# Kernel tuning notes

Measured on AMD Instinct MI355X. Metric: run time of the kernel, lower is better.

Reference implementation:

```python
import math
import jax, jax.numpy as jnp
import numpy as np

B, S, D, H, FF = 2, 2048, 1024, 16, 4096
HD = D // H  # head dim = 64
EPS = 1e-12


def setup_inputs() -> dict:
    key = jax.random.key(0)
    ks = jax.random.split(key, 16)
    w = lambda k, shape: (jax.random.normal(k, shape, jnp.float32) * 0.02)
    return {
        "hidden_states": jax.random.normal(ks[0], (B, S, D), jnp.float32),
        "attention_mask": jnp.zeros((B, 1, 1, S), jnp.float32),
        "wq": w(ks[1], (D, D)), "bq": jnp.zeros((D,), jnp.float32),
        "wk": w(ks[2], (D, D)), "bk": jnp.zeros((D,), jnp.float32),
        "wv": w(ks[3], (D, D)), "bv": jnp.zeros((D,), jnp.float32),
        "wo": w(ks[4], (D, D)), "bo": jnp.zeros((D,), jnp.float32),
        "w1": w(ks[5], (D, FF)), "b1": jnp.zeros((FF,), jnp.float32),
        "w2": w(ks[6], (FF, D)), "b2": jnp.zeros((D,), jnp.float32),
        "g1": jnp.ones((D,), jnp.float32), "be1": jnp.zeros((D,), jnp.float32),
        "g2": jnp.ones((D,), jnp.float32), "be2": jnp.zeros((D,), jnp.float32),
    }


def _layernorm(x, g, b):
    mu = jnp.mean(x, axis=-1, keepdims=True)
    var = jnp.mean(jnp.square(x - mu), axis=-1, keepdims=True)
    return (x - mu) * jax.lax.rsqrt(var + EPS) * g + b


def _gelu_erf(x):
    # x * 0.5 * (1 + erf(x / sqrt(2)))  -- exact erf gelu as in source
    return x * 0.5 * (1.0 + jax.lax.erf(x / math.sqrt(2.0)))


def _attention(x, mask, wq, bq, wk, bk, wv, bv, wo, bo):
    b, s, d = x.shape
    split = lambda t: t.reshape(b, s, H, HD).transpose(0, 2, 1, 3)  # [b,h,s,hd]
    q = split(x @ wq + bq)
    k = split(x @ wk + bk)
    v = split(x @ wv + bv)
    scores = jnp.einsum("bhqd,bhkd->bhqk", q, k) / math.sqrt(HD)
    scores = scores + mask  # broadcast [b,1,1,s]
    probs = jax.nn.softmax(scores, axis=-1)
    ctx = jnp.einsum("bhqk,bhkd->bhqd", probs, v)
    ctx = ctx.transpose(0, 2, 1, 3).reshape(b, s, d)
    return ctx @ wo + bo


def reference(hidden_states, attention_mask, wq, bq, wk, bk, wv, bv, wo, bo,
              w1, b1, w2, b2, g1, be1, g2, be2):
    # prenorm transformer layer (dropout = identity in eval)
    residual = hidden_states
    h = _layernorm(hidden_states, g1, be1)
    attn = _attention(h, attention_mask, wq, bq, wk, bk, wv, bv, wo, bo)
    h = residual + attn
    residual = h
    h2 = _layernorm(h, g2, be2)
    ff = _gelu_erf(h2 @ w1 + b1) @ w2 + b2
    return residual + ff
```

## Files before the change

kernel.cpp:

```cpp
#include <hip/hip_runtime.h>
#include <hip/hip_bf16.h>
#include <math.h>


#define BB 2
#define SS 2048
#define DD 1024
#define HH 16
#define HDIM 64
#define FFD 4096
#define NTOK (BB*SS)
#define LOG2E 1.4426950408889634f

typedef __attribute__((ext_vector_type(8))) short bf16x8;
typedef __attribute__((ext_vector_type(4))) float f32x4;
typedef __attribute__((ext_vector_type(16))) float f32x16;
typedef __attribute__((ext_vector_type(4))) unsigned int u32x4;

#if __has_builtin(__builtin_amdgcn_exp2f)
#define EXP2(x) __builtin_amdgcn_exp2f(x)
#else
#define EXP2(x) exp2f(x)
#endif

__device__ __forceinline__ void gl_lds16(const void* g, void* l) {
  __builtin_amdgcn_global_load_lds(
      (const __attribute__((address_space(1))) unsigned int*)g,
      (__attribute__((address_space(3))) unsigned int*)l, 16, 0, 0);
}

__device__ __forceinline__ short f2bf(float f) {
  unsigned int u = __builtin_bit_cast(unsigned int, f);
  unsigned int r = (u + 0x7fffu + ((u >> 16) & 1u)) >> 16;
  return (short)r;
}
__device__ __forceinline__ float bf2f(short s) {
  return __builtin_bit_cast(float, ((unsigned)(unsigned short)s) << 16);
}
__device__ __forceinline__ unsigned pk2(float lo, float hi) {
  unsigned r;
  asm("v_cvt_pk_bf16_f32 %0, %1, %2" : "=v"(r) : "v"(lo), "v"(hi));
  return r;
}

__global__ __launch_bounds__(256) void convT(const float* __restrict__ w,
                                             __hip_bfloat16* __restrict__ wt,
                                             int K, int N) {
  __shared__ float tile[32][33];
  int k0 = blockIdx.y * 32, n0 = blockIdx.x * 32;
  int tx = threadIdx.x & 31, ty = threadIdx.x >> 5;
#pragma unroll
  for (int i = 0; i < 4; ++i) {
    int r = ty + i * 8;
    tile[r][tx] = w[(size_t)(k0 + r) * N + n0 + tx];
  }
  __syncthreads();
#pragma unroll
  for (int i = 0; i < 4; ++i) {
    int r = ty + i * 8;
    wt[(size_t)(n0 + r) * K + k0 + tx] = __float2bfloat16(tile[tx][r]);
  }
}

__global__ __launch_bounds__(256) void ln_bf16(const float* __restrict__ x,
                                               const float* __restrict__ g,
                                               const float* __restrict__ be,
                                               __hip_bfloat16* __restrict__ out) {
  int w = threadIdx.x >> 6, lane = threadIdx.x & 63;
  int row = blockIdx.x * 4 + w;
  const float* xr = x + (size_t)row * DD;
  float4 v[4];
  float sum = 0.f, sq = 0.f;
#pragma unroll
  for (int i = 0; i < 4; ++i) {
    v[i] = *(const float4*)(xr + lane * 4 + i * 256);
    sum += v[i].x + v[i].y + v[i].z + v[i].w;
    sq += v[i].x * v[i].x + v[i].y * v[i].y + v[i].z * v[i].z + v[i].w * v[i].w;
  }
#pragma unroll
  for (int off = 1; off < 64; off <<= 1) {
    sum += __shfl_xor(sum, off);
    sq += __shfl_xor(sq, off);
  }
  float mu = sum * (1.f / 1024.f);
  float var = sq * (1.f / 1024.f) - mu * mu;
  float rs = rsqrtf(var + 1e-12f);
  __hip_bfloat16* orow = out + (size_t)row * DD;
#pragma unroll
  for (int i = 0; i < 4; ++i) {
    int c = lane * 4 + i * 256;
    float4 gg = *(const float4*)(g + c);
    float4 bb = *(const float4*)(be + c);
    short4 o;
    o.x = f2bf((v[i].x - mu) * rs * gg.x + bb.x);
    o.y = f2bf((v[i].y - mu) * rs * gg.y + bb.y);
    o.z = f2bf((v[i].z - mu) * rs * gg.z + bb.z);
    o.w = f2bf((v[i].w - mu) * rs * gg.w + bb.w);
    *(short4*)((short*)orow + c) = o;
  }
}

template <int EPI>
__global__ __launch_bounds__(256, 4) void gemm_bt(
    const __hip_bfloat16* __restrict__ A, const __hip_bfloat16* __restrict__ BT,
    const float* __restrict__ bA, const float* __restrict__ bB,
    const float* __restrict__ bC,
    void* __restrict__ C0, void* __restrict__ C1, void* __restrict__ C2,
    int M, int N, int K, int kSplit) {
  __shared__ __align__(16) char smem[34816];
  short* As = (short*)smem;
  short* Bs = (short*)(smem + 8192);
  const int t = threadIdx.x, lane = t & 63, w = t >> 6;
  const int m0 = blockIdx.y * 128, n0 = blockIdx.x * 128;
  const int wm = (w >> 1) * 64, wn = (w & 1) * 64;
  const int row16 = lane & 15, grp = lane >> 4;
  const int arow = t >> 2, achunk = t & 3;
  f32x4 acc[4][4] = {};

  const int steps = K >> 5;
  const int z = blockIdx.z;
  const int sBeg = (z * steps) / kSplit, sEnd = ((z + 1) * steps) / kSplit;

  for (int s = sBeg; s < sEnd; ++s) {
    const int kt = s << 5;
    __syncthreads();
#pragma unroll
    for (int j = 0; j < 2; ++j) {
      int r = arow + j * 64;
      gl_lds16(A + (size_t)(m0 + r) * K + kt + achunk * 8,
               (char*)As + r * 64 + achunk * 16);
      gl_lds16(BT + (size_t)(n0 + r) * K + kt + achunk * 8,
               (char*)Bs + r * 64 + achunk * 16);
    }
    __syncthreads();
    bf16x8 af[4], bfr[4];
#pragma unroll
    for (int f = 0; f < 4; ++f) {
      af[f] = *(const bf16x8*)((const char*)As + (wm + f * 16 + row16) * 64 + grp * 16);
      bfr[f] = *(const bf16x8*)((const char*)Bs + (wn + f * 16 + row16) * 64 + grp * 16);
    }
#pragma unroll
    for (int mf = 0; mf < 4; ++mf)
#pragma unroll
      for (int nf = 0; nf < 4; ++nf)
        acc[mf][nf] =
            __builtin_amdgcn_mfma_f32_16x16x32_bf16(af[mf], bfr[nf], acc[mf][nf], 0, 0, 0);
  }

  __syncthreads();

  if constexpr (EPI == 5) {
    if (n0 >= 2048) {
#pragma unroll
      for (int nf = 0; nf < 4; ++nf) {
        int vloc = wn + nf * 16 + row16;
        float bv = bC[n0 - 2048 + vloc];
#pragma unroll
        for (int mf = 0; mf < 4; ++mf) {
          int tloc = wm + mf * 16 + grp * 4;
          f32x4 a = acc[mf][nf];
          *(uint2*)(smem + vloc * 272 + tloc * 2) =
              make_uint2(pk2(a[0] + bv, a[1] + bv), pk2(a[2] + bv, a[3] + bv));
        }
      }
      __syncthreads();
      int vrBase = ((m0 >> 11) << 10) + (n0 - 2048);
      int mcol = m0 & 2047;
#pragma unroll
      for (int i = 0; i < 8; ++i) {
        int c = t + i * 256;
        int vr = c >> 4, tc = c & 15;
        u32x4 vv = *(const u32x4*)(smem + vr * 272 + tc * 16);
        *(u32x4*)((__hip_bfloat16*)C2 + (size_t)(vrBase + vr) * 2048 + mcol + tc * 8) = vv;
      }
      return;
    }
  }

  __hip_bfloat16* outP = nullptr;
  int ldO = N, colB = n0;
  const float* bp = nullptr;
  if constexpr (EPI == 1) { outP = (__hip_bfloat16*)C0; bp = bA; }
  if constexpr (EPI == 5) {
    const bool isK = n0 >= 1024;
    outP = (__hip_bfloat16*)(isK ? C1 : C0);
    bp = isK ? bB : bA;
    ldO = 1024; colB = n0 & 1023;
  }
  if constexpr (EPI == 7) outP = (__hip_bfloat16*)C0 + (size_t)z * 4194304ull;
  if constexpr (EPI == 8)
    outP = (__hip_bfloat16*)C0 + ((z == 0) ? 0ull : ((z == 1) ? 4194304ull : 12582912ull));

#pragma unroll
  for (int nf = 0; nf < 4; ++nf) {
    int nn = wn + nf * 16 + row16;
    float bv = bp ? bp[colB + nn] : 0.f;
#pragma unroll
    for (int mf = 0; mf < 4; ++mf) {
      int mloc = wm + mf * 16 + grp * 4;
      f32x4 a = acc[mf][nf];
#pragma unroll
      for (int r = 0; r < 4; ++r) {
        float v = a[r] + bv;
        if constexpr (EPI == 1)
          v = 0.5f * v * (1.0f + erff(v * 0.70710678118654752f));
        *(short*)(smem + (mloc + r) * 272 + nn * 2) = f2bf(v);
      }
    }
  }
  __syncthreads();
#pragma unroll
  for (int i = 0; i < 8; ++i) {
    int c = t + i * 256;
    int mmr = c >> 4, nc = c & 15;
    u32x4 vv = *(const u32x4*)(smem + mmr * 272 + nc * 16);
    *(u32x4*)(outP + (size_t)(m0 + mmr) * ldO + colB + nc * 8) = vv;
  }
}

__global__ __launch_bounds__(256) void reduce3(const __hip_bfloat16* __restrict__ p0,
                                               const __hip_bfloat16* __restrict__ p1,
                                               const __hip_bfloat16* __restrict__ p2,
                                               const float* __restrict__ h1,
                                               const float* __restrict__ b2,
                                               float* __restrict__ out) {
  int idx = (blockIdx.x * 256 + threadIdx.x) * 8;
  int n = idx & 1023;
  bf16x8 a = *(const bf16x8*)(p0 + idx);
  bf16x8 b = *(const bf16x8*)(p1 + idx);
  bf16x8 c = *(const bf16x8*)(p2 + idx);
  float4 hA = *(const float4*)(h1 + idx), hB = *(const float4*)(h1 + idx + 4);
  float4 bA = *(const float4*)(b2 + n), bB = *(const float4*)(b2 + n + 4);
  float o[8];
#pragma unroll
  for (int j = 0; j < 8; ++j) o[j] = bf2f(a[j]) + bf2f(b[j]) + bf2f(c[j]);
  float4 r0 = make_float4(o[0] + hA.x + bA.x, o[1] + hA.y + bA.y,
                          o[2] + hA.z + bA.z, o[3] + hA.w + bA.w);
  float4 r1 = make_float4(o[4] + hB.x + bB.x, o[5] + hB.y + bB.y,
                          o[6] + hB.z + bB.z, o[7] + hB.w + bB.w);
  *(float4*)(out + idx) = r0;
  *(float4*)(out + idx + 4) = r1;
}

__global__ __launch_bounds__(256) void reduce4(const __hip_bfloat16* __restrict__ p0,
                                               const __hip_bfloat16* __restrict__ p1,
                                               const __hip_bfloat16* __restrict__ p2,
                                               const __hip_bfloat16* __restrict__ p3,
                                               const float* __restrict__ x,
                                               const float* __restrict__ bo,
                                               float* __restrict__ out) {
  int idx = (blockIdx.x * 256 + threadIdx.x) * 8;
  int n = idx & 1023;
  bf16x8 a = *(const bf16x8*)(p0 + idx);
  bf16x8 b = *(const bf16x8*)(p1 + idx);
  bf16x8 c = *(const bf16x8*)(p2 + idx);
  bf16x8 d = *(const bf16x8*)(p3 + idx);
  float4 hA = *(const float4*)(x + idx), hB = *(const float4*)(x + idx + 4);
  float4 bA = *(const float4*)(bo + n), bB = *(const float4*)(bo + n + 4);
  float o[8];
#pragma unroll
  for (int j = 0; j < 8; ++j)
    o[j] = (bf2f(a[j]) + bf2f(b[j])) + (bf2f(c[j]) + bf2f(d[j]));
  float4 r0 = make_float4(o[0] + hA.x + bA.x, o[1] + hA.y + bA.y,
                          o[2] + hA.z + bA.z, o[3] + hA.w + bA.w);
  float4 r1 = make_float4(o[4] + hB.x + bB.x, o[5] + hB.y + bB.y,
                          o[6] + hB.z + bB.z, o[7] + hB.w + bB.w);
  *(float4*)(out + idx) = r0;
  *(float4*)(out + idx + 4) = r1;
}

__global__ __launch_bounds__(512) void flash_attn2(
    const __hip_bfloat16* __restrict__ Q,
    const __hip_bfloat16* __restrict__ Kg,
    const __hip_bfloat16* __restrict__ VTg,
    const float* __restrict__ mask,
    __hip_bfloat16* __restrict__ pctx0,
    __hip_bfloat16* __restrict__ pctx1,
    float2* __restrict__ ml) {
  __shared__ __align__(16) char lds[33280];
  const int t = threadIdx.x, lane = t & 63, w = t >> 6;
  const int l31 = lane & 31, hi = lane >> 5;
  const int q0 = blockIdx.x * 256;
  const int bh = blockIdx.y, b = bh >> 4, h = bh & 15;
  const int z = blockIdx.z;
  const int kvBase = z * (SS / 2);
  __hip_bfloat16* pctx = z ? pctx1 : pctx0;
  const int qrow = q0 + w * 32 + l31;

  bf16x8 qf[4];
  {
    const __hip_bfloat16* qp = Q + ((size_t)(b * SS + qrow)) * DD + h * HDIM + hi * 8;
    qf[0] = *(const bf16x8*)(qp);
    qf[1] = *(const bf16x8*)(qp + 16);
    qf[2] = *(const bf16x8*)(qp + 32);
    qf[3] = *(const bf16x8*)(qp + 48);
  }
  f32x16 ctx0 = {}, ctx1 = {};
  float m = -1e30f, l = 0.f, mC = -1.44e30f;

  auto stage = [&](int buf, int kv0) {
    int r = t >> 3, c = t & 7;
    gl_lds16(Kg + ((size_t)(b * SS + kv0 + r)) * DD + h * HDIM + ((c ^ (r & 7)) * 8),
             lds + buf * 8192 + t * 16);
    gl_lds16(VTg + ((size_t)(bh * 64 + r)) * 2048 + kv0 + ((c ^ (r & 7)) * 8),
             lds + 16384 + buf * 8192 + t * 16);
    if (t < 64) *(float*)(lds + 32768 + buf * 256 + t * 4) = mask[b * SS + kv0 + t];
  };

  stage(0, kvBase);
  const int NIT = SS / 128;
  for (int it = 0; it < NIT; ++it) {
    __syncthreads();
    if (it + 1 < NIT) stage((it + 1) & 1, kvBase + (it + 1) * 64);
    const char* Kb = lds + (it & 1) * 8192;
    const char* Vb = lds + 16384 + (it & 1) * 8192;
    const float* mk = (const float*)(lds + 32768 + (it & 1) * 256);

    f32x16 s0 = {}, s1 = {};
#pragma unroll
    for (int kc = 0; kc < 4; ++kc) {
      int c = kc * 2 + hi;
      int r0 = l31, r1 = 32 + l31;
      bf16x8 ka0 = *(const bf16x8*)(Kb + r0 * 128 + ((c ^ (r0 & 7)) << 4));
      bf16x8 ka1 = *(const bf16x8*)(Kb + r1 * 128 + ((c ^ (r1 & 7)) << 4));
      s0 = __builtin_amdgcn_mfma_f32_32x32x16_bf16(ka0, qf[kc], s0, 0, 0, 0);
      s1 = __builtin_amdgcn_mfma_f32_32x32x16_bf16(ka1, qf[kc], s1, 0, 0, 0);
    }
#pragma unroll
    for (int g = 0; g < 4; ++g) {
      float4 mg0 = *(const float4*)(mk + g * 8 + hi * 4);
      float4 mg1 = *(const float4*)(mk + 32 + g * 8 + hi * 4);
      const float* m0p = (const float*)&mg0;
      const float* m1p = (const float*)&mg1;
#pragma unroll
      for (int i = 0; i < 4; ++i) {
        s0[g * 4 + i] = fmaf(s0[g * 4 + i], 0.125f, m0p[i]);
        s1[g * 4 + i] = fmaf(s1[g * 4 + i], 0.125f, m1p[i]);
      }
    }
    float pmax;
    {
      f32x16 q8;
#pragma unroll
      for (int r = 0; r < 16; ++r) q8[r] = fmaxf(s0[r], s1[r]);
#pragma unroll
      for (int r = 0; r < 8; ++r) q8[r] = fmaxf(q8[r], q8[r + 8]);
#pragma unroll
      for (int r = 0; r < 4; ++r) q8[r] = fmaxf(q8[r], q8[r + 4]);
      pmax = fmaxf(fmaxf(q8[0], q8[1]), fmaxf(q8[2], q8[3]));
      pmax = fmaxf(pmax, __shfl_xor(pmax, 32));
    }
    if (__any(pmax > m + 8.0f)) {
      float mnew = fmaxf(m, pmax);
      float fac = EXP2((m - mnew) * LOG2E);
      l *= fac;
#pragma unroll
      for (int r = 0; r < 16; ++r) { ctx0[r] *= fac; ctx1[r] *= fac; }
      m = mnew;
      mC = m * LOG2E;
    }
    float rsA = 0.f, rsB = 0.f;
#pragma unroll
    for (int r = 0; r < 16; ++r) {
      s0[r] = EXP2(fmaf(s0[r], LOG2E, -mC));
      s1[r] = EXP2(fmaf(s1[r], LOG2E, -mC));
      rsA += s0[r];
      rsB += s1[r];
    }
    rsA += rsB;
    rsA += __shfl_xor(rsA, 32);
    l += rsA;

    unsigned W0[8], W1[8];
#pragma unroll
    for (int g = 0; g < 4; ++g) {
      W0[g * 2] = pk2(s0[g * 4 + 0], s0[g * 4 + 1]);
      W0[g * 2 + 1] = pk2(s0[g * 4 + 2], s0[g * 4 + 3]);
      W1[g * 2] = pk2(s1[g * 4 + 0], s1[g * 4 + 1]);
      W1[g * 2 + 1] = pk2(s1[g * 4 + 2], s1[g * 4 + 3]);
    }
    unsigned swA0 = __shfl_xor(hi ? W0[0] : W0[2], 32);
    unsigned swA1 = __shfl_xor(hi ? W0[1] : W0[3], 32);
    unsigned swB0 = __shfl_xor(hi ? W0[4] : W0[6], 32);
    unsigned swB1 = __shfl_xor(hi ? W0[5] : W0[7], 32);
    unsigned swC0 = __shfl_xor(hi ? W1[0] : W1[2], 32);
    unsigned swC1 = __shfl_xor(hi ? W1[1] : W1[3], 32);
    unsigned swD0 = __shfl_xor(hi ? W1[4] : W1[6], 32);
    unsigned swD1 = __shfl_xor(hi ? W1[5] : W1[7], 32);
    u32x4 pb[4];
    pb[0] = hi ? (u32x4){swA0, swA1, W0[2], W0[3]} : (u32x4){W0[0], W0[1], swA0, swA1};
    pb[1] = hi ? (u32x4){swB0, swB1, W0[6], W0[7]} : (u32x4){W0[4], W0[5], swB0, swB1};
    pb[2] = hi ? (u32x4){swC0, swC1, W1[2], W1[3]} : (u32x4){W1[0], W1[1], swC0, swC1};
    pb[3] = hi ? (u32x4){swD0, swD1, W1[6], W1[7]} : (u32x4){W1[4], W1[5], swD0, swD1};

#pragma unroll
    for (int kc = 0; kc < 4; ++kc) {
      bf16x8 pbf = __builtin_bit_cast(bf16x8, pb[kc]);
      int c = kc * 2 + hi;
      int r0 = l31, r1 = 32 + l31;
      bf16x8 va0 = *(const bf16x8*)(Vb + r0 * 128 + ((c ^ (r0 & 7)) << 4));
      bf16x8 va1 = *(const bf16x8*)(Vb + r1 * 128 + ((c ^ (r1 & 7)) << 4));
      ctx0 = __builtin_amdgcn_mfma_f32_32x32x16_bf16(va0, pbf, ctx0, 0, 0, 0);
      ctx1 = __builtin_amdgcn_mfma_f32_32x32x16_bf16(va1, pbf, ctx1, 0, 0, 0);
    }
  }

  if (hi == 0) ml[((size_t)z * NTOK + b * SS + qrow) * HH + h] = make_float2(m, l);

  __syncthreads();
  {
    int row = w * 32 + l31;
#pragma unroll
    for (int dt = 0; dt < 2; ++dt) {
#pragma unroll
      for (int g = 0; g < 4; ++g) {
        unsigned lo2 = dt ? pk2(ctx1[g * 4 + 0], ctx1[g * 4 + 1]) : pk2(ctx0[g * 4 + 0], ctx0[g * 4 + 1]);
        unsigned hi2 = dt ? pk2(ctx1[g * 4 + 2], ctx1[g * 4 + 3]) : pk2(ctx0[g * 4 + 2], ctx0[g * 4 + 3]);
        int c = dt * 4 + g;
        *(uint2*)(lds + row * 128 + ((c ^ (row & 7)) << 4) + hi * 8) = make_uint2(lo2, hi2);
      }
    }
  }
  __syncthreads();
  {
    int r = t >> 1;
    size_t tok = (size_t)(b * SS + q0 + r);
#pragma unroll
    for (int i = 0; i < 4; ++i) {
      int c = (t & 1) * 4 + i;
      u32x4 vv = *(const u32x4*)(lds + r * 128 + ((c ^ (r & 7)) << 4));
      *(u32x4*)((short*)pctx + tok * DD + h * HDIM + c * 8) = vv;
    }
  }
}

__global__ __launch_bounds__(256) void mergeAttn(
    const __hip_bfloat16* __restrict__ p0, const __hip_bfloat16* __restrict__ p1,
    const float2* __restrict__ ml, __hip_bfloat16* __restrict__ out) {
  int tok = blockIdx.x, tid = threadIdx.x;
  int h = tid >> 4;
  float2 a = ml[(size_t)tok * HH + h];
  float2 b = ml[(size_t)(NTOK + tok) * HH + h];
  float M = fmaxf(a.x, b.x);
  float w0 = EXP2((a.x - M) * LOG2E), w1 = EXP2((b.x - M) * LOG2E);
  float inv = 1.0f / (w0 * a.y + w1 * b.y);
  w0 *= inv; w1 *= inv;
  size_t idx = (size_t)tok * DD + tid * 4;
  short4 c0 = *(const short4*)((const short*)p0 + idx);
  short4 c1 = *(const short4*)((const short*)p1 + idx);
  unsigned lo = pk2(w0 * bf2f(c0.x) + w1 * bf2f(c1.x),
                    w0 * bf2f(c0.y) + w1 * bf2f(c1.y));
  unsigned hi2 = pk2(w0 * bf2f(c0.z) + w1 * bf2f(c1.z),
                     w0 * bf2f(c0.w) + w1 * bf2f(c1.w));
  *(uint2*)((short*)out + idx) = make_uint2(lo, hi2);
}

extern "C" void kernel_launch(void* const* d_in, const int* in_sizes, int n_in,
                              void* d_out, int out_size, void* d_ws, size_t ws_size,
                              hipStream_t stream) {
  const float* x = (const float*)d_in[0];
  const float* mask = (const float*)d_in[1];
  const float* wq = (const float*)d_in[2];
  const float* bq = (const float*)d_in[3];
  const float* wk = (const float*)d_in[4];
  const float* bk = (const float*)d_in[5];
  const float* wv = (const float*)d_in[6];
  const float* bv = (const float*)d_in[7];
  const float* wo = (const float*)d_in[8];
  const float* bo = (const float*)d_in[9];
  const float* w1 = (const float*)d_in[10];
  const float* b1 = (const float*)d_in[11];
  const float* w2 = (const float*)d_in[12];
  const float* b2 = (const float*)d_in[13];
  const float* g1 = (const float*)d_in[14];
  const float* be1 = (const float*)d_in[15];
  const float* g2 = (const float*)d_in[16];
  const float* be2 = (const float*)d_in[17];

  char* ws = (char*)d_ws;
  const size_t MB = 1024ull * 1024ull;
  __hip_bfloat16* wqkvT = (__hip_bfloat16*)(ws + 0 * MB);
  __hip_bfloat16* woT = (__hip_bfloat16*)(ws + 6 * MB);
  __hip_bfloat16* w1T = (__hip_bfloat16*)(ws + 8 * MB);
  __hip_bfloat16* w2T = (__hip_bfloat16*)(ws + 16 * MB);
  __hip_bfloat16* xn = (__hip_bfloat16*)(ws + 24 * MB);
  __hip_bfloat16* qb = (__hip_bfloat16*)(ws + 32 * MB);
  __hip_bfloat16* kb = (__hip_bfloat16*)(ws + 40 * MB);
  __hip_bfloat16* vtb = (__hip_bfloat16*)(ws + 48 * MB);
  __hip_bfloat16* ctxb = (__hip_bfloat16*)(ws + 56 * MB);
  float* h1 = (float*)(ws + 64 * MB);
  __hip_bfloat16* h2 = xn;
  __hip_bfloat16* a1 = qb;
  __hip_bfloat16* pctx0 = (__hip_bfloat16*)(ws + 24 * MB);
  __hip_bfloat16* pctx1 = (__hip_bfloat16*)(ws + 64 * MB);
  float2* mlbuf = (float2*)(ws + 72 * MB);

  convT<<<dim3(32, 32), 256, 0, stream>>>(wq, wqkvT, 1024, 1024);
  convT<<<dim3(32, 32), 256, 0, stream>>>(wk, wqkvT + 1024 * 1024, 1024, 1024);
  convT<<<dim3(32, 32), 256, 0, stream>>>(wv, wqkvT + 2 * 1024 * 1024, 1024, 1024);
  convT<<<dim3(32, 32), 256, 0, stream>>>(wo, woT, 1024, 1024);
  convT<<<dim3(128, 32), 256, 0, stream>>>(w1, w1T, 1024, 4096);
  convT<<<dim3(32, 128), 256, 0, stream>>>(w2, w2T, 4096, 1024);

  ln_bf16<<<1024, 256, 0, stream>>>(x, g1, be1, xn);

  gemm_bt<5><<<dim3(24, 32), 256, 0, stream>>>(
      xn, wqkvT, bq, bk, bv, qb, kb, vtb, NTOK, 3072, 1024, 1);

  flash_attn2<<<dim3(8, 32, 2), 512, 0, stream>>>(qb, kb, vtb, mask,
                                                  pctx0, pctx1, mlbuf);
  mergeAttn<<<4096, 256, 0, stream>>>(pctx0, pctx1, mlbuf, ctxb);

  gemm_bt<7><<<dim3(8, 32, 4), 256, 0, stream>>>(
      ctxb, woT, nullptr, nullptr, nullptr, ws + 24 * MB, nullptr, nullptr,
      NTOK, 1024, 1024, 4);

  reduce4<<<2048, 256, 0, stream>>>((__hip_bfloat16*)(ws + 24 * MB),
                                    (__hip_bfloat16*)(ws + 32 * MB),
                                    (__hip_bfloat16*)(ws + 40 * MB),
                                    (__hip_bfloat16*)(ws + 48 * MB),
                                    x, bo, h1);

  ln_bf16<<<1024, 256, 0, stream>>>(h1, g2, be2, h2);

  gemm_bt<1><<<dim3(32, 32), 256, 0, stream>>>(
      h2, w1T, b1, nullptr, nullptr, a1, nullptr, nullptr, NTOK, FFD, 1024, 1);

  gemm_bt<8><<<dim3(8, 32, 3), 256, 0, stream>>>(
      a1, w2T, nullptr, nullptr, nullptr, ws, nullptr, nullptr,
      NTOK, 1024, FFD, 3);

  reduce3<<<2048, 256, 0, stream>>>((__hip_bfloat16*)(ws + 0 * MB),
                                    (__hip_bfloat16*)(ws + 8 * MB),
                                    (__hip_bfloat16*)(ws + 24 * MB),
                                    h1, b2, (float*)d_out);
}
```

Baseline: 287.9 us.

## Triple-buffer GEMM LDS tiles with async global-to-LDS prefetch two stages ahead

Replaces the single-buffered GEMM main loop (sync, load, sync, compute) with a three-stage LDS ring buffer. Global-to-LDS loads for tile t+2 are issued before the MFMAs of tile t, with explicit vmcnt waits and a single barrier per iteration. The aim is to hide global memory latency behind the matrix math and halve the barriers. In exchange LDS per block grows to 48KB and launch bounds drop to 3 blocks per CU, which lowers occupancy.

```diff
diff --git a/kernel.cpp b/kernel.cpp
--- a/kernel.cpp
+++ b/kernel.cpp
@@ -22,6 +22,12 @@
 #else
 #define EXP2(x) exp2f(x)
 #endif
+
+#define BAR __builtin_amdgcn_s_barrier
+#define SCB __builtin_amdgcn_sched_barrier
+#define VM4 asm volatile("s_waitcnt vmcnt(4)" ::: "memory")
+#define VM0 asm volatile("s_waitcnt vmcnt(0)" ::: "memory")
+#define LGK0 asm volatile("s_waitcnt lgkmcnt(0)" ::: "memory")
 
 __device__ __forceinline__ void gl_lds16(const void* g, void* l) {
   __builtin_amdgcn_global_load_lds(
@@ -101,15 +107,13 @@
 }
 
 template <int EPI>
-__global__ __launch_bounds__(256, 4) void gemm_bt(
+__global__ __launch_bounds__(256, 3) void gemm_bt(
     const __hip_bfloat16* __restrict__ A, const __hip_bfloat16* __restrict__ BT,
     const float* __restrict__ bA, const float* __restrict__ bB,
     const float* __restrict__ bC,
     void* __restrict__ C0, void* __restrict__ C1, void* __restrict__ C2,
     int M, int N, int K, int kSplit) {
-  __shared__ __align__(16) char smem[34816];
-  short* As = (short*)smem;
-  short* Bs = (short*)(smem + 8192);
+  __shared__ __align__(16) char smem[49152];
   const int t = threadIdx.x, lane = t & 63, w = t >> 6;
   const int m0 = blockIdx.y * 128, n0 = blockIdx.x * 128;
   const int wm = (w >> 1) * 64, wn = (w & 1) * 64;
@@ -120,31 +124,52 @@
   const int steps = K >> 5;
   const int z = blockIdx.z;
   const int sBeg = (z * steps) / kSplit, sEnd = ((z + 1) * steps) / kSplit;
-
-  for (int s = sBeg; s < sEnd; ++s) {
-    const int kt = s << 5;
-    __syncthreads();
-#pragma unroll
-    for (int j = 0; j < 2; ++j) {
-      int r = arow + j * 64;
-      gl_lds16(A + (size_t)(m0 + r) * K + kt + achunk * 8,
-               (char*)As + r * 64 + achunk * 16);
-      gl_lds16(BT + (size_t)(n0 + r) * K + kt + achunk * 8,
-               (char*)Bs + r * 64 + achunk * 16);
-    }
-    __syncthreads();
+  const int NT = sEnd - sBeg;
+
+  const __hip_bfloat16* gA0 = A + (size_t)(m0 + arow) * K + achunk * 8;
+  const __hip_bfloat16* gA1 = A + (size_t)(m0 + arow + 64) * K + achunk * 8;
+  const __hip_bfloat16* gB0 = BT + (size_t)(n0 + arow) * K + achunk * 8;
+  const __hip_bfloat16* gB1 = BT + (size_t)(n0 + arow + 64) * K + achunk * 8;
+  char* ldsA0 = smem + arow * 64 + achunk * 16;
+  char* ldsA1 = smem + (arow + 64) * 64 + achunk * 16;
+  char* ldsB0 = smem + 8192 + arow * 64 + achunk * 16;
+  char* ldsB1 = smem + 8192 + (arow + 64) * 64 + achunk * 16;
+
+  auto stage = [&](int st, int buf) {
+    int kt = (sBeg + st) << 5;
+    char* o = (char*)0 + buf * 16384;
+    gl_lds16(gA0 + kt, ldsA0 + (size_t)(o - (char*)0));
+    gl_lds16(gA1 + kt, ldsA1 + (size_t)(o - (char*)0));
+    gl_lds16(gB0 + kt, ldsB0 + (size_t)(o - (char*)0));
+    gl_lds16(gB1 + kt, ldsB1 + (size_t)(o - (char*)0));
+  };
+
+  stage(0, 0);
+  if (NT > 1) stage(1, 1);
+  VM4; SCB(0);
+  BAR(); SCB(0);
+
+  for (int tt = 0; tt < NT; ++tt) {
+    const char* bufR = smem + (tt % 3) * 16384;
     bf16x8 af[4], bfr[4];
 #pragma unroll
     for (int f = 0; f < 4; ++f) {
-      af[f] = *(const bf16x8*)((const char*)As + (wm + f * 16 + row16) * 64 + grp * 16);
-      bfr[f] = *(const bf16x8*)((const char*)Bs + (wn + f * 16 + row16) * 64 + grp * 16);
-    }
+      af[f] = *(const bf16x8*)(bufR + (wm + f * 16 + row16) * 64 + grp * 16);
+      bfr[f] = *(const bf16x8*)(bufR + 8192 + (wn + f * 16 + row16) * 64 + grp * 16);
+    }
+    const bool more = (tt + 2 < NT);
+    if (more) stage(tt + 2, (tt + 2) % 3);
+    LGK0; SCB(0);
 #pragma unroll
     for (int mf = 0; mf < 4; ++mf)
 #pragma unroll
       for (int nf = 0; nf < 4; ++nf)
         acc[mf][nf] =
             __builtin_amdgcn_mfma_f32_16x16x32_bf16(af[mf], bfr[nf], acc[mf][nf], 0, 0, 0);
+    SCB(0);
+    if (more) { VM4; } else { VM0; }
+    SCB(0);
+    BAR(); SCB(0);
   }
 
   __syncthreads();
```

Measured after the change: 283.4 us. No clear change (-1.5%).

## Fuse residual reduction with LayerNorm, batch weight transposes, use tanh GELU

Applied to the files above, without the earlier changes.

Merges the four-way split-K reduction of the attention output projection with the second LayerNorm, so h1 is no longer re-read by a separate kernel. Combines the four square weight transposes into one launch using blockIdx.z. Replaces the erf GELU in the FFN epilogue with a tanh-style approximation built on exp2. The tanh approximation adds small numerical deviation from the exact erf GELU, and the fused LayerNorm computes variance as E[x^2]-mu^2.

```diff
diff --git a/kernel.cpp b/kernel.cpp
--- a/kernel.cpp
+++ b/kernel.cpp
@@ -42,6 +42,12 @@
   asm("v_cvt_pk_bf16_f32 %0, %1, %2" : "=v"(r) : "v"(lo), "v"(hi));
   return r;
 }
+__device__ __forceinline__ float gelu_fast(float v) {
+  float v2 = v * v;
+  float u = v * (0.7978845608028654f + 0.03567740814183427f * v2);
+  float e = EXP2(u * 2.8853900817779268f);
+  return v * (1.0f - 1.0f / (e + 1.0f));
+}
 
 __global__ __launch_bounds__(256) void convT(const float* __restrict__ w,
                                              __hip_bfloat16* __restrict__ wt,
@@ -59,6 +65,30 @@
   for (int i = 0; i < 4; ++i) {
     int r = ty + i * 8;
     wt[(size_t)(n0 + r) * K + k0 + tx] = __float2bfloat16(tile[tx][r]);
+  }
+}
+
+__global__ __launch_bounds__(256) void convT4(const float* __restrict__ w0,
+                                              const float* __restrict__ w1,
+                                              const float* __restrict__ w2,
+                                              const float* __restrict__ w3,
+                                              __hip_bfloat16* __restrict__ out) {
+  __shared__ float tile[32][33];
+  int z = blockIdx.z;
+  const float* w = (z == 0) ? w0 : (z == 1) ? w1 : (z == 2) ? w2 : w3;
+  __hip_bfloat16* wt = out + (size_t)z * 1024 * 1024;
+  int k0 = blockIdx.y * 32, n0 = blockIdx.x * 32;
+  int tx = threadIdx.x & 31, ty = threadIdx.x >> 5;
+#pragma unroll
+  for (int i = 0; i < 4; ++i) {
+    int r = ty + i * 8;
+    tile[r][tx] = w[(size_t)(k0 + r) * 1024 + n0 + tx];
+  }
+  __syncthreads();
+#pragma unroll
+  for (int i = 0; i < 4; ++i) {
+    int r = ty + i * 8;
+    wt[(size_t)(n0 + r) * 1024 + k0 + tx] = __float2bfloat16(tile[tx][r]);
   }
 }
 
@@ -202,8 +232,7 @@
 #pragma unroll
       for (int r = 0; r < 4; ++r) {
         float v = a[r] + bv;
-        if constexpr (EPI == 1)
-          v = 0.5f * v * (1.0f + erff(v * 0.70710678118654752f));
+        if constexpr (EPI == 1) v = gelu_fast(v);
         *(short*)(smem + (mloc + r) * 272 + nn * 2) = f2bf(v);
       }
     }
@@ -242,31 +271,54 @@
   *(float4*)(out + idx + 4) = r1;
 }
 
-__global__ __launch_bounds__(256) void reduce4(const __hip_bfloat16* __restrict__ p0,
-                                               const __hip_bfloat16* __restrict__ p1,
-                                               const __hip_bfloat16* __restrict__ p2,
-                                               const __hip_bfloat16* __restrict__ p3,
-                                               const float* __restrict__ x,
-                                               const float* __restrict__ bo,
-                                               float* __restrict__ out) {
-  int idx = (blockIdx.x * 256 + threadIdx.x) * 8;
-  int n = idx & 1023;
+__global__ __launch_bounds__(256) void reduce4_ln(
+    const __hip_bfloat16* __restrict__ p0, const __hip_bfloat16* __restrict__ p1,
+    const __hip_bfloat16* __restrict__ p2, const __hip_bfloat16* __restrict__ p3,
+    const float* __restrict__ x, const float* __restrict__ bo,
+    const float* __restrict__ g, const float* __restrict__ be,
+    float* __restrict__ h1, __hip_bfloat16* __restrict__ h2) {
+  __shared__ float red[4][2];
+  const int tid = threadIdx.x;
+  const int rowHalf = tid >> 7, tloc = tid & 127, wv = tid >> 6;
+  const size_t idx = ((size_t)blockIdx.x * 2 + rowHalf) * 1024 + tloc * 8;
+  const int n = tloc * 8;
   bf16x8 a = *(const bf16x8*)(p0 + idx);
   bf16x8 b = *(const bf16x8*)(p1 + idx);
   bf16x8 c = *(const bf16x8*)(p2 + idx);
   bf16x8 d = *(const bf16x8*)(p3 + idx);
-  float4 hA = *(const float4*)(x + idx), hB = *(const float4*)(x + idx + 4);
+  float4 xA = *(const float4*)(x + idx), xB = *(const float4*)(x + idx + 4);
   float4 bA = *(const float4*)(bo + n), bB = *(const float4*)(bo + n + 4);
   float o[8];
 #pragma unroll
   for (int j = 0; j < 8; ++j)
     o[j] = (bf2f(a[j]) + bf2f(b[j])) + (bf2f(c[j]) + bf2f(d[j]));
-  float4 r0 = make_float4(o[0] + hA.x + bA.x, o[1] + hA.y + bA.y,
-                          o[2] + hA.z + bA.z, o[3] + hA.w + bA.w);
-  float4 r1 = make_float4(o[4] + hB.x + bB.x, o[5] + hB.y + bB.y,
-                          o[6] + hB.z + bB.z, o[7] + hB.w + bB.w);
-  *(float4*)(out + idx) = r0;
-  *(float4*)(out + idx + 4) = r1;
+  o[0] += xA.x + bA.x; o[1] += xA.y + bA.y; o[2] += xA.z + bA.z; o[3] += xA.w + bA.w;
+  o[4] += xB.x + bB.x; o[5] += xB.y + bB.y; o[6] += xB.z + bB.z; o[7] += xB.w + bB.w;
+  *(float4*)(h1 + idx) = make_float4(o[0], o[1], o[2], o[3]);
+  *(float4*)(h1 + idx + 4) = make_float4(o[4], o[5], o[6], o[7]);
+  float s = 0.f, sq = 0.f;
+#pragma unroll
+  for (int j = 0; j < 8; ++j) { s += o[j]; sq += o[j] * o[j]; }
+#pragma unroll
+  for (int off = 1; off < 64; off <<= 1) {
+    s += __shfl_xor(s, off);
+    sq += __shfl_xor(sq, off);
+  }
+  if ((tid & 63) == 0) { red[wv][0] = s; red[wv][1] = sq; }
+  __syncthreads();
+  float S = red[rowHalf * 2][0] + red[rowHalf * 2 + 1][0];
+  float SQ = red[rowHalf * 2][1] + red[rowHalf * 2 + 1][1];
+  float mu = S * (1.f / 1024.f);
+  float var = SQ * (1.f / 1024.f) - mu * mu;
+  float rs = rsqrtf(var + 1e-12f);
+  float4 gA = *(const float4*)(g + n), gB = *(const float4*)(g + n + 4);
+  float4 eA = *(const float4*)(be + n), eB = *(const float4*)(be + n + 4);
+  u32x4 pkd;
+  pkd[0] = pk2((o[0] - mu) * rs * gA.x + eA.x, (o[1] - mu) * rs * gA.y + eA.y);
+  pkd[1] = pk2((o[2] - mu) * rs * gA.z + eA.z, (o[3] - mu) * rs * gA.w + eA.w);
+  pkd[2] = pk2((o[4] - mu) * rs * gB.x + eB.x, (o[5] - mu) * rs * gB.y + eB.y);
+  pkd[3] = pk2((o[6] - mu) * rs * gB.z + eB.z, (o[7] - mu) * rs * gB.w + eB.w);
+  *(u32x4*)((short*)h2 + idx) = pkd;
 }
 
 __global__ __launch_bounds__(512) void flash_attn2(
@@ -495,10 +547,7 @@
   __hip_bfloat16* pctx1 = (__hip_bfloat16*)(ws + 64 * MB);
   float2* mlbuf = (float2*)(ws + 72 * MB);
 
-  convT<<<dim3(32, 32), 256, 0, stream>>>(wq, wqkvT, 1024, 1024);
-  convT<<<dim3(32, 32), 256, 0, stream>>>(wk, wqkvT + 1024 * 1024, 1024, 1024);
-  convT<<<dim3(32, 32), 256, 0, stream>>>(wv, wqkvT + 2 * 1024 * 1024, 1024, 1024);
-  convT<<<dim3(32, 32), 256, 0, stream>>>(wo, woT, 1024, 1024);
+  convT4<<<dim3(32, 32, 4), 256, 0, stream>>>(wq, wk, wv, wo, wqkvT);
   convT<<<dim3(128, 32), 256, 0, stream>>>(w1, w1T, 1024, 4096);
   convT<<<dim3(32, 128), 256, 0, stream>>>(w2, w2T, 4096, 1024);
 
@@ -515,13 +564,11 @@
       ctxb, woT, nullptr, nullptr, nullptr, ws + 24 * MB, nullptr, nullptr,
       NTOK, 1024, 1024, 4);
 
-  reduce4<<<2048, 256, 0, stream>>>((__hip_bfloat16*)(ws + 24 * MB),
-                                    (__hip_bfloat16*)(ws + 32 * MB),
-                                    (__hip_bfloat16*)(ws + 40 * MB),
-                                    (__hip_bfloat16*)(ws + 48 * MB),
-                                    x, bo, h1);
-
-  ln_bf16<<<1024, 256, 0, stream>>>(h1, g2, be2, h2);
+  reduce4_ln<<<2048, 256, 0, stream>>>((__hip_bfloat16*)(ws + 24 * MB),
+                                       (__hip_bfloat16*)(ws + 32 * MB),
+                                       (__hip_bfloat16*)(ws + 40 * MB),
+                                       (__hip_bfloat16*)(ws + 48 * MB),
+                                       x, bo, g2, be2, h1, h2);
 
   gemm_bt<1><<<dim3(32, 32), 256, 0, stream>>>(
       h2, w1T, b1, nullptr, nullptr, a1, nullptr, nullptr, NTOK, FFD, 1024, 1);
```

Measured after the change: 273.6 us. -5.0%, faster.
